# Optimization experiments

Hardware: AMD Instinct MI355X
Metric: run time of the kernel (lower is better)

## Reference

```python
import jax, jax.numpy as jnp
import numpy as np

N, E, D, R = 50000, 800000, 64, 65


def setup_inputs() -> dict:
    key = jax.random.key(0)
    ks = jax.random.split(key, 8)
    x = jax.random.normal(ks[0], (N, D), dtype=jnp.float32)
    src = jax.random.randint(ks[1], (E,), 0, N, dtype=jnp.int32)
    dst = jax.random.randint(ks[2], (E,), 0, N, dtype=jnp.int32)
    edge_type = jax.random.randint(ks[3], (E,), 0, R, dtype=jnp.int32)
    s = 1.0 / np.sqrt(D)
    W1 = jax.random.normal(ks[4], (R, D, D), dtype=jnp.float32) * s
    Wl1 = jax.random.normal(ks[5], (D, D), dtype=jnp.float32) * s
    W2 = jax.random.normal(ks[6], (R, D, D), dtype=jnp.float32) * s
    Wl2 = jax.random.normal(ks[7], (D, D), dtype=jnp.float32) * s
    return {"x": x, "src": src, "dst": dst, "edge_type": edge_type,
            "W1": W1, "Wl1": Wl1, "W2": W2, "Wl2": Wl2}


def _rgcn_layer(x, src, dst, edge_type, W, Wl):
    # x: [N, D_in], W: [R, D_in, D_out], Wl: [D_in, D_out]
    n = x.shape[0]
    r = W.shape[0]
    # per-relation transform of all node features: [R, N, D_out]
    xw = jnp.einsum('nd,rdh->rnh', x, W)
    # gather transformed source feature for each edge by its relation: [E, D_out]
    msg = xw[edge_type, src]
    # mean aggregation per (destination node, relation) as in PyG RGCNConv
    key = dst.astype(jnp.int32) * r + edge_type
    cnt = jax.ops.segment_sum(jnp.ones(key.shape, x.dtype), key, num_segments=n * r)
    norm = 1.0 / jnp.maximum(cnt[key], 1.0)  # [E]
    agg = jax.ops.segment_sum(msg * norm[:, None], dst, num_segments=n)  # [N, D_out]
    # self-loop linear term (self_loop_weights in original module)
    out = agg + x @ Wl
    # activation; dropout is identity in eval mode; batch norm disabled
    return jax.nn.relu(out)


def reference(x, src, dst, edge_type, W1, Wl1, W2, Wl2):
    h = _rgcn_layer(x, src, dst, edge_type, W1, Wl1)
    h = _rgcn_layer(h, src, dst, edge_type, W2, Wl2)
    return h
```

## Files before the change

kernel.cpp:

```cpp
#include <hip/hip_runtime.h>

typedef __attribute__((ext_vector_type(8))) short bf16x8;
typedef __attribute__((ext_vector_type(4))) float f32x4;

#define RFL(v) __builtin_amdgcn_readfirstlane(v)

constexpr int D = 64;
constexpr int SEG = 64;
constexpr int CSTR = 16;

__device__ inline unsigned short f2bf(float f) {
  unsigned u = __float_as_uint(f);
  u += 0x7fff + ((u >> 16) & 1);
  return (unsigned short)(u >> 16);
}
__device__ inline float bflo(unsigned u) { return __uint_as_float(u << 16); }
__device__ inline float bfhi(unsigned u) { return __uint_as_float(u & 0xffff0000u); }

__global__ __launch_bounds__(256) void count_kernel(
    const int* __restrict__ dst, const int* __restrict__ et,
    int* __restrict__ bcnt, int* __restrict__ deg, int E, int R, int nbE) {
  __shared__ int lh[128];
  int t = threadIdx.x;
  if (t < 128) lh[t] = 0;
  __syncthreads();
  int e = blockIdx.x * 256 + t;
  if (e < E) {
    atomicAdd(&deg[(long)dst[e] * CSTR], 1);
    atomicAdd(&lh[et[e]], 1);
  }
  __syncthreads();
  if (t < R) bcnt[t * nbE + blockIdx.x] = lh[t];
}

__global__ __launch_bounds__(256) void scanA_kernel(
    const int* __restrict__ arr, int* __restrict__ bsum, int n, int stride) {
  __shared__ int s[256];
  int t = threadIdx.x;
  int i = blockIdx.x * 256 + t;
  s[t] = (i < n) ? arr[(long)i * stride] : 0;
  __syncthreads();
  for (int o = 128; o > 0; o >>= 1) {
    if (t < o) s[t] += s[t + o];
    __syncthreads();
  }
  if (t == 0) bsum[blockIdx.x] = s[0];
}

__global__ __launch_bounds__(256) void scanB_kernel(int* __restrict__ bsum, int nb) {
  __shared__ int s[256];
  __shared__ int carry;
  int t = threadIdx.x;
  if (t == 0) carry = 0;
  __syncthreads();
  for (int base = 0; base < nb; base += 256) {
    int i = base + t;
    int v = (i < nb) ? bsum[i] : 0;
    s[t] = v;
    __syncthreads();
    for (int o = 1; o < 256; o <<= 1) {
      int u = (t >= o) ? s[t - o] : 0;
      __syncthreads();
      s[t] += u;
      __syncthreads();
    }
    if (i < nb) bsum[i] = carry + s[t] - v;
    __syncthreads();
    if (t == 0) carry += s[255];
    __syncthreads();
  }
}

__global__ __launch_bounds__(256) void scanC_pref_kernel(
    const int* __restrict__ arr, const int* __restrict__ bsum,
    int* __restrict__ pref, int n) {
  __shared__ int s[256];
  int t = threadIdx.x;
  int i = blockIdx.x * 256 + t;
  int v = (i < n) ? arr[i] : 0;
  s[t] = v;
  __syncthreads();
  for (int o = 1; o < 256; o <<= 1) {
    int u = (t >= o) ? s[t - o] : 0;
    __syncthreads();
    s[t] += u;
    __syncthreads();
  }
  int excl = bsum[blockIdx.x] + s[t] - v;
  if (i < n) pref[i] = excl;
  if (i == n - 1) pref[n] = excl + v;
}

__global__ __launch_bounds__(256) void scanC_deg_kernel(
    const int* __restrict__ deg, const int* __restrict__ bsum,
    int* __restrict__ dstoff, int* __restrict__ cur2, int N) {
  __shared__ int s[256];
  int t = threadIdx.x;
  int i = blockIdx.x * 256 + t;
  int v = (i < N) ? deg[(long)i * CSTR] : 0;
  s[t] = v;
  __syncthreads();
  for (int o = 1; o < 256; o <<= 1) {
    int u = (t >= o) ? s[t - o] : 0;
    __syncthreads();
    s[t] += u;
    __syncthreads();
  }
  int excl = bsum[blockIdx.x] + s[t] - v;
  if (i < N) { dstoff[i] = excl; cur2[(long)i * CSTR] = excl; }
  if (i == N - 1) dstoff[N] = excl + v;
}

__global__ void prefix_kernel(const int* __restrict__ prefE,
                              int* __restrict__ cursor, int nbE, int R) {
  __shared__ int sc[128];
  int l = threadIdx.x;
  int c = 0;
  if (l < R) {
    int tot = prefE[(l + 1) * nbE] - prefE[l * nbE];
    c = (tot + SEG - 1) & ~(SEG - 1);
  }
  sc[l] = c;
  __syncthreads();
  for (int ofs = 1; ofs < 128; ofs <<= 1) {
    int v = (l >= ofs) ? sc[l - ofs] : 0;
    __syncthreads();
    sc[l] += v;
    __syncthreads();
  }
  if (l < R) cursor[l] = sc[l] - c;
}

__global__ void wrel_kernel(const int* __restrict__ prefE, const int* __restrict__ cursor,
                            int* __restrict__ wrel, int nbE, int R) {
  int r = threadIdx.x;
  if (r >= R) return;
  int tot = prefE[(r + 1) * nbE] - prefE[r * nbE];
  int w0 = cursor[r] >> 6;
  int nw = (tot + SEG - 1) >> 6;
  for (int w = 0; w < nw; ++w) wrel[w0 + w] = r;
}

__global__ __launch_bounds__(256) void scatter_kernel(
    const int* __restrict__ src, const int* __restrict__ dst, const int* __restrict__ et,
    const int* __restrict__ cursor, const int* __restrict__ prefE,
    int* __restrict__ cur2, int2* __restrict__ eidx,
    int E, int R, int nbE) {
  __shared__ int lh[128];
  __shared__ int lbase[128];
  int t = threadIdx.x, b = blockIdx.x;
  if (t < R) {
    lh[t] = 0;
    lbase[t] = cursor[t] + prefE[t * nbE + b] - prefE[t * nbE];
  }
  __syncthreads();
  int e = b * 256 + t;
  if (e < E) {
    int r = et[e], s = src[e], d = dst[e];
    int lr = atomicAdd(&lh[r], 1);
    int jd = atomicAdd(&cur2[(long)d * CSTR], 1);
    int pos = lbase[r] + lr;
    eidx[pos] = make_int2(s, jd);
  }
}

__global__ __launch_bounds__(256) void cvt_x_kernel(
    const float* __restrict__ x, unsigned short* __restrict__ xb, int n) {
  int i = blockIdx.x * 256 + threadIdx.x;
  if (i < n) xb[i] = f2bf(x[i]);
}

__global__ __launch_bounds__(256) void cvt_w_kernel(
    const float* __restrict__ W, unsigned short* __restrict__ WT, int total) {
  int i = blockIdx.x * 256 + threadIdx.x;
  if (i >= total) return;
  int n = i & 63, k = (i >> 6) & 63, r = i >> 12;
  WT[(r << 12) + (n << 6) + k] = f2bf(W[(r << 12) + (k << 6) + n]);
}

__global__ __launch_bounds__(256) __attribute__((amdgpu_waves_per_eu(1, 4)))
void msg_kernel(const unsigned short* __restrict__ xb,
                const unsigned short* __restrict__ WT,
                const int2* __restrict__ eidx, const int* __restrict__ wrel,
                unsigned int* __restrict__ msgp, int* __restrict__ relrow, int nwaves) {
  const int lane = (int)threadIdx.x & 63;
  const int l15 = lane & 15;
  const int q = lane >> 4;
  const int wave = blockIdx.x * 4 + ((int)threadIdx.x >> 6);
  if (wave >= nwaves) return;
  const long base = (long)wave * SEG;
  const int r = wrel[wave];
  const unsigned short* wb = WT + ((long)r << 12);
  bf16x8 Bf[4][2];
#pragma unroll
  for (int nt = 0; nt < 4; ++nt)
#pragma unroll
    for (int kh = 0; kh < 2; ++kh)
      Bf[nt][kh] = *(const bf16x8*)(wb + (nt * 16 + l15) * 64 + kh * 32 + q * 8);
#pragma unroll
  for (int t = 0; t < 4; ++t) {
    int2 rec = eidx[base + t * 16 + l15];
    if (relrow && lane < 16 && rec.y >= 0) relrow[rec.y] = r;
    const unsigned short* xr = xb + ((long)max(rec.x, 0) << 6);
    bf16x8 A0 = *(const bf16x8*)(xr + q * 8);
    bf16x8 A1 = *(const bf16x8*)(xr + 32 + q * 8);
    f32x4 acc0 = (f32x4)0.0f, acc1 = (f32x4)0.0f, acc2 = (f32x4)0.0f, acc3 = (f32x4)0.0f;
    acc0 = __builtin_amdgcn_mfma_f32_16x16x32_bf16(A0, Bf[0][0], acc0, 0, 0, 0);
    acc0 = __builtin_amdgcn_mfma_f32_16x16x32_bf16(A1, Bf[0][1], acc0, 0, 0, 0);
    acc1 = __builtin_amdgcn_mfma_f32_16x16x32_bf16(A0, Bf[1][0], acc1, 0, 0, 0);
    acc1 = __builtin_amdgcn_mfma_f32_16x16x32_bf16(A1, Bf[1][1], acc1, 0, 0, 0);
    acc2 = __builtin_amdgcn_mfma_f32_16x16x32_bf16(A0, Bf[2][0], acc2, 0, 0, 0);
    acc2 = __builtin_amdgcn_mfma_f32_16x16x32_bf16(A1, Bf[2][1], acc2, 0, 0, 0);
    acc3 = __builtin_amdgcn_mfma_f32_16x16x32_bf16(A0, Bf[3][0], acc3, 0, 0, 0);
    acc3 = __builtin_amdgcn_mfma_f32_16x16x32_bf16(A1, Bf[3][1], acc3, 0, 0, 0);
#pragma unroll
    for (int rg = 0; rg < 4; ++rg) {
      int row = q * 4 + rg;
      int jd = __shfl(rec.y, row);
      if (jd >= 0) {
        unsigned p0 = (unsigned)f2bf(acc0[rg]) | ((unsigned)f2bf(acc1[rg]) << 16);
        unsigned p1 = (unsigned)f2bf(acc2[rg]) | ((unsigned)f2bf(acc3[rg]) << 16);
        unsigned int* mp = msgp + (long)jd * 32;
        mp[l15] = p0;
        mp[16 + l15] = p1;
      }
    }
  }
}

__global__ __launch_bounds__(256) void agg_kernel(
    const unsigned int* __restrict__ msgp, const int* __restrict__ dstoff,
    const int* __restrict__ relrow, float* __restrict__ agg, int N) {
  __shared__ int rsh[4][256];
  __shared__ float fsh[4][256];
  const int wv = (int)threadIdx.x >> 6;
  const int lane = (int)threadIdx.x & 63;
  const int j = lane & 31;
  const int half = lane >> 5;
  const int d = blockIdx.x * 4 + wv;
  if (d >= N) return;
  const int off = dstoff[d], end = dstoff[d + 1];
  const int deg = end - off;
  float aLo = 0.f, aHi = 0.f;
  if (deg > 0 && deg <= 256) {
    const int nit = (deg + 63) >> 6;
    int cl[4];
    for (int it = 0; it < nit; ++it) {
      int l = it * 64 + lane;
      if (l < deg) rsh[wv][l] = relrow[off + l];
    }
    __threadfence_block();
    for (int it = 0; it < nit; ++it) {
      int l = it * 64 + lane;
      if (l < deg) {
        int rv = rsh[wv][l];
        int c = 0;
        for (int m = 0; m < deg; ++m) c += (rsh[wv][m] == rv) ? 1 : 0;
        cl[it] = c;
      }
    }
    for (int it = 0; it < nit; ++it) {
      int l = it * 64 + lane;
      if (l < deg) fsh[wv][l] = 1.0f / (float)cl[it];
    }
    __threadfence_block();
    float a0 = 0.f, a1 = 0.f, b0 = 0.f, b1 = 0.f;
    int i = off + half;
    for (; i + 2 < end; i += 4) {
      float w0 = fsh[wv][i - off];
      float w1 = fsh[wv][i + 2 - off];
      unsigned u0 = msgp[(long)i * 32 + j];
      unsigned u1 = msgp[(long)(i + 2) * 32 + j];
      a0 = fmaf(w0, bflo(u0), a0);
      a1 = fmaf(w0, bfhi(u0), a1);
      b0 = fmaf(w1, bflo(u1), b0);
      b1 = fmaf(w1, bfhi(u1), b1);
    }
    if (i < end) {
      float w0 = fsh[wv][i - off];
      unsigned u0 = msgp[(long)i * 32 + j];
      a0 = fmaf(w0, bflo(u0), a0);
      a1 = fmaf(w0, bfhi(u0), a1);
    }
    aLo = a0 + b0;
    aHi = a1 + b1;
  } else if (deg > 256) {
    for (int i = off + half; i < end; i += 2) {
      int rv = relrow[i];
      int c = 0;
      for (int m = off; m < end; ++m) c += (relrow[m] == rv) ? 1 : 0;
      float w = 1.0f / (float)c;
      unsigned u0 = msgp[(long)i * 32 + j];
      aLo = fmaf(w, bflo(u0), aLo);
      aHi = fmaf(w, bfhi(u0), aHi);
    }
  }
  aLo += __shfl_xor(aLo, 32);
  aHi += __shfl_xor(aHi, 32);
  if (half == 0) {
    int colLo = (j < 16) ? j : j + 16;
    agg[(long)d * D + colLo] = aLo;
    agg[(long)d * D + colLo + 16] = aHi;
  }
}

__global__ __launch_bounds__(256) void selfloop_kernel(
    const unsigned short* __restrict__ xbin, const unsigned short* __restrict__ WTl,
    const float* __restrict__ agg, float* __restrict__ out,
    unsigned short* __restrict__ hb, int N) {
  const int lane = (int)threadIdx.x & 63;
  const int l15 = lane & 15;
  const int q = lane >> 4;
  const int wave = blockIdx.x * 4 + ((int)threadIdx.x >> 6);
  const int base = wave * 64;
  if (base >= N) return;
  bf16x8 Bf[4][2];
#pragma unroll
  for (int nt = 0; nt < 4; ++nt)
#pragma unroll
    for (int kh = 0; kh < 2; ++kh)
      Bf[nt][kh] = *(const bf16x8*)(WTl + (nt * 16 + l15) * 64 + kh * 32 + q * 8);
#pragma unroll
  for (int t = 0; t < 4; ++t) {
    const int row0 = base + t * 16;
    if (row0 >= N) break;
    const int m = min(row0 + l15, N - 1);
    const unsigned short* xr = xbin + ((long)m << 6);
    bf16x8 A0 = *(const bf16x8*)(xr + q * 8);
    bf16x8 A1 = *(const bf16x8*)(xr + 32 + q * 8);
    f32x4 acc[4];
#pragma unroll
    for (int nt = 0; nt < 4; ++nt) {
#pragma unroll
      for (int rg = 0; rg < 4; ++rg) {
        int node = row0 + q * 4 + rg;
        acc[nt][rg] = (node < N) ? agg[(long)node * D + nt * 16 + l15] : 0.0f;
      }
    }
#pragma unroll
    for (int nt = 0; nt < 4; ++nt) {
      acc[nt] = __builtin_amdgcn_mfma_f32_16x16x32_bf16(A0, Bf[nt][0], acc[nt], 0, 0, 0);
      acc[nt] = __builtin_amdgcn_mfma_f32_16x16x32_bf16(A1, Bf[nt][1], acc[nt], 0, 0, 0);
    }
#pragma unroll
    for (int rg = 0; rg < 4; ++rg) {
      int node = row0 + q * 4 + rg;
      if (node < N) {
#pragma unroll
        for (int nt = 0; nt < 4; ++nt) {
          float v = fmaxf(acc[nt][rg], 0.0f);
          out[(long)node * D + nt * 16 + l15] = v;
          if (hb) hb[(long)node * D + nt * 16 + l15] = f2bf(v);
        }
      }
    }
  }
}

extern "C" void kernel_launch(void* const* d_in, const int* in_sizes, int n_in,
                              void* d_out, int out_size, void* d_ws, size_t ws_size,
                              hipStream_t stream) {
  const float* x   = (const float*)d_in[0];
  const int* src   = (const int*)d_in[1];
  const int* dst   = (const int*)d_in[2];
  const int* et    = (const int*)d_in[3];
  const float* W1  = (const float*)d_in[4];
  const float* Wl1 = (const float*)d_in[5];
  const float* W2  = (const float*)d_in[6];
  const float* Wl2 = (const float*)d_in[7];
  float* out = (float*)d_out;

  const int N = in_sizes[0] / D;
  const int E = in_sizes[1];
  const int R = in_sizes[4] / (D * D);

  const int Ecap = ((E + SEG - 1) & ~(SEG - 1)) + R * SEG;
  const int nwaves = Ecap / SEG;
  const int nbN = (N + 255) / 256;
  const int nbE = (E + 255) / 256;
  const int nBC = R * nbE;
  const int nbBC = (nBC + 255) / 256;
  const int nbMax = (nbBC > nbN) ? nbBC : nbN;

  char* ws = (char*)d_ws;
  size_t off = 0;
  auto alloc = [&](size_t bytes) -> void* {
    void* p = (void*)(ws + off);
    off += (bytes + 255) & ~(size_t)255;
    return p;
  };
  int*   cursor = (int*)alloc((size_t)R * sizeof(int));
  int*   deg    = (int*)alloc((size_t)N * CSTR * sizeof(int));
  int*   cur2   = (int*)alloc((size_t)N * CSTR * sizeof(int));
  int*   bcnt   = (int*)alloc((size_t)nBC * sizeof(int));
  int*   prefE  = (int*)alloc((size_t)(nBC + 1) * sizeof(int));
  int*   bsum   = (int*)alloc((size_t)nbMax * sizeof(int));
  int*   dstoff = (int*)alloc((size_t)(N + 1) * sizeof(int));
  int*   relrow = (int*)alloc((size_t)E * sizeof(int));
  int*   wrel   = (int*)alloc((size_t)nwaves * sizeof(int));
  int2*  eidx   = (int2*)alloc((size_t)(Ecap + SEG) * sizeof(int2));
  unsigned int* msgp = (unsigned int*)alloc((size_t)E * 32 * sizeof(unsigned int));
  float* agg    = (float*)alloc((size_t)N * D * sizeof(float));
  unsigned short* xb  = (unsigned short*)alloc((size_t)N * D * sizeof(unsigned short));
  unsigned short* hb  = (unsigned short*)alloc((size_t)N * D * sizeof(unsigned short));
  unsigned short* WT1 = (unsigned short*)alloc((size_t)R * D * D * sizeof(unsigned short));
  unsigned short* WT2 = (unsigned short*)alloc((size_t)R * D * D * sizeof(unsigned short));
  unsigned short* WTl1 = (unsigned short*)alloc((size_t)D * D * sizeof(unsigned short));
  unsigned short* WTl2 = (unsigned short*)alloc((size_t)D * D * sizeof(unsigned short));
  (void)ws_size; (void)n_in; (void)out_size;

  const int msg_blocks = (nwaves + 3) / 4;
  const int agg_blocks = (N + 3) / 4;
  const int sl_waves = (N + 63) / 64;
  const int sl_blocks = (sl_waves + 3) / 4;
  const int wtot = R * D * D;

  hipMemsetAsync(deg, 0, (size_t)N * CSTR * sizeof(int), stream);
  hipMemsetAsync(wrel, 0, (size_t)nwaves * sizeof(int), stream);
  hipMemsetAsync(eidx, 0xFF, (size_t)(Ecap + SEG) * sizeof(int2), stream);
  count_kernel<<<nbE, 256, 0, stream>>>(dst, et, bcnt, deg, E, R, nbE);
  scanA_kernel<<<nbBC, 256, 0, stream>>>(bcnt, bsum, nBC, 1);
  scanB_kernel<<<1, 256, 0, stream>>>(bsum, nbBC);
  scanC_pref_kernel<<<nbBC, 256, 0, stream>>>(bcnt, bsum, prefE, nBC);
  prefix_kernel<<<1, 128, 0, stream>>>(prefE, cursor, nbE, R);
  wrel_kernel<<<1, 128, 0, stream>>>(prefE, cursor, wrel, nbE, R);
  scanA_kernel<<<nbN, 256, 0, stream>>>(deg, bsum, N, CSTR);
  scanB_kernel<<<1, 256, 0, stream>>>(bsum, nbN);
  scanC_deg_kernel<<<nbN, 256, 0, stream>>>(deg, bsum, dstoff, cur2, N);
  scatter_kernel<<<nbE, 256, 0, stream>>>(src, dst, et, cursor, prefE, cur2,
                                          eidx, E, R, nbE);
  cvt_x_kernel<<<(N * D + 255) / 256, 256, 0, stream>>>(x, xb, N * D);
  cvt_w_kernel<<<(wtot + 255) / 256, 256, 0, stream>>>(W1, WT1, wtot);
  cvt_w_kernel<<<(wtot + 255) / 256, 256, 0, stream>>>(W2, WT2, wtot);
  cvt_w_kernel<<<(D * D + 255) / 256, 256, 0, stream>>>(Wl1, WTl1, D * D);
  cvt_w_kernel<<<(D * D + 255) / 256, 256, 0, stream>>>(Wl2, WTl2, D * D);

  msg_kernel<<<msg_blocks, 256, 0, stream>>>(xb, WT1, eidx, wrel, msgp, relrow, nwaves);
  agg_kernel<<<agg_blocks, 256, 0, stream>>>(msgp, dstoff, relrow, agg, N);
  selfloop_kernel<<<sl_blocks, 256, 0, stream>>>(xb, WTl1, agg, out, hb, N);

  msg_kernel<<<msg_blocks, 256, 0, stream>>>(hb, WT2, eidx, wrel, msgp, nullptr, nwaves);
  agg_kernel<<<agg_blocks, 256, 0, stream>>>(msgp, dstoff, relrow, agg, N);
  selfloop_kernel<<<sl_blocks, 256, 0, stream>>>(hb, WTl2, agg, out, nullptr, N);
}
```

Before: 364.0 us.

## Fuse prefix and wrel kernels, use nontemporal message stores, drop waves_per_eu hint

Merges the relation prefix scan and the wave-to-relation fill into one kernel, removing one tiny launch. The message and relrow scatter stores in msg_kernel become nontemporal so these streaming writes are meant to bypass cache retention. The waves_per_eu attribute is removed from msg_kernel, which lets the compiler choose its own register budget and occupancy. The nontemporal writes may slow the following agg_kernel if its msgp reads would otherwise have hit in cache.

```diff
diff --git a/kernel.cpp b/kernel.cpp
--- a/kernel.cpp
+++ b/kernel.cpp
@@ -111,8 +111,9 @@
   if (i == N - 1) dstoff[N] = excl + v;
 }
 
-__global__ void prefix_kernel(const int* __restrict__ prefE,
-                              int* __restrict__ cursor, int nbE, int R) {
+__global__ void prefix_wrel_kernel(const int* __restrict__ prefE,
+                                   int* __restrict__ cursor, int* __restrict__ wrel,
+                                   int nbE, int R) {
   __shared__ int sc[128];
   int l = threadIdx.x;
   int c = 0;
@@ -128,17 +129,13 @@
     sc[l] += v;
     __syncthreads();
   }
-  if (l < R) cursor[l] = sc[l] - c;
-}
-
-__global__ void wrel_kernel(const int* __restrict__ prefE, const int* __restrict__ cursor,
-                            int* __restrict__ wrel, int nbE, int R) {
-  int r = threadIdx.x;
-  if (r >= R) return;
-  int tot = prefE[(r + 1) * nbE] - prefE[r * nbE];
-  int w0 = cursor[r] >> 6;
-  int nw = (tot + SEG - 1) >> 6;
-  for (int w = 0; w < nw; ++w) wrel[w0 + w] = r;
+  if (l < R) {
+    int cur = sc[l] - c;
+    cursor[l] = cur;
+    int w0 = cur >> 6;
+    int nw = c >> 6;
+    for (int w = 0; w < nw; ++w) wrel[w0 + w] = l;
+  }
 }
 
 __global__ __launch_bounds__(256) void scatter_kernel(
@@ -178,7 +175,7 @@
   WT[(r << 12) + (n << 6) + k] = f2bf(W[(r << 12) + (k << 6) + n]);
 }
 
-__global__ __launch_bounds__(256) __attribute__((amdgpu_waves_per_eu(1, 4)))
+__global__ __launch_bounds__(256)
 void msg_kernel(const unsigned short* __restrict__ xb,
                 const unsigned short* __restrict__ WT,
                 const int2* __restrict__ eidx, const int* __restrict__ wrel,
@@ -200,7 +197,8 @@
 #pragma unroll
   for (int t = 0; t < 4; ++t) {
     int2 rec = eidx[base + t * 16 + l15];
-    if (relrow && lane < 16 && rec.y >= 0) relrow[rec.y] = r;
+    if (relrow && lane < 16 && rec.y >= 0)
+      __builtin_nontemporal_store(r, &relrow[rec.y]);
     const unsigned short* xr = xb + ((long)max(rec.x, 0) << 6);
     bf16x8 A0 = *(const bf16x8*)(xr + q * 8);
     bf16x8 A1 = *(const bf16x8*)(xr + 32 + q * 8);
@@ -221,8 +219,8 @@
         unsigned p0 = (unsigned)f2bf(acc0[rg]) | ((unsigned)f2bf(acc1[rg]) << 16);
         unsigned p1 = (unsigned)f2bf(acc2[rg]) | ((unsigned)f2bf(acc3[rg]) << 16);
         unsigned int* mp = msgp + (long)jd * 32;
-        mp[l15] = p0;
-        mp[16 + l15] = p1;
+        __builtin_nontemporal_store(p0, &mp[l15]);
+        __builtin_nontemporal_store(p1, &mp[16 + l15]);
       }
     }
   }
@@ -422,8 +420,7 @@
   scanA_kernel<<<nbBC, 256, 0, stream>>>(bcnt, bsum, nBC, 1);
   scanB_kernel<<<1, 256, 0, stream>>>(bsum, nbBC);
   scanC_pref_kernel<<<nbBC, 256, 0, stream>>>(bcnt, bsum, prefE, nBC);
-  prefix_kernel<<<1, 128, 0, stream>>>(prefE, cursor, nbE, R);
-  wrel_kernel<<<1, 128, 0, stream>>>(prefE, cursor, wrel, nbE, R);
+  prefix_wrel_kernel<<<1, 128, 0, stream>>>(prefE, cursor, wrel, nbE, R);
   scanA_kernel<<<nbN, 256, 0, stream>>>(deg, bsum, N, CSTR);
   scanB_kernel<<<1, 256, 0, stream>>>(bsum, nbN);
   scanC_deg_kernel<<<nbN, 256, 0, stream>>>(deg, bsum, dstoff, cur2, N);
```

Measured after the change: 376.0 us. 1.03x slower.
